# Kernel optimization log

Measured on AMD Instinct MI355X. Metric: run time of the kernel, lower is better.

Reference implementation:

```python
import jax, jax.numpy as jnp
import numpy as np

B, S, HID, H = 4, 1024, 1024, 16
D = HID // H


def setup_inputs() -> dict:
    key = jax.random.key(0)
    ks = jax.random.split(key, 4)
    scale = 0.02
    return {
        "hidden_states": jax.random.normal(ks[0], (B, S, HID), dtype=jnp.float32),
        "attention_mask": jnp.ones((B, S), dtype=jnp.int32),
        "layer_head_mask": jnp.ones((H,), dtype=jnp.float32),
        "Wq": jax.random.normal(ks[1], (HID, HID), dtype=jnp.float32) * scale,
        "bq": jnp.zeros((HID,), dtype=jnp.float32),
        "Wk": jax.random.normal(ks[2], (HID, HID), dtype=jnp.float32) * scale,
        "bk": jnp.zeros((HID,), dtype=jnp.float32),
        "Wv": jax.random.normal(ks[3], (HID, HID), dtype=jnp.float32) * scale,
        "bv": jnp.zeros((HID,), dtype=jnp.float32),
    }


def reference(hidden_states, attention_mask, layer_head_mask, Wq, bq, Wk, bk, Wv, bv):
    b, s, _ = hidden_states.shape
    # QKV projections, split heads: [B,S,H,D]
    q = (hidden_states @ Wq + bq).reshape(b, s, H, D)
    k = (hidden_states @ Wk + bk).reshape(b, s, H, D)
    v = (hidden_states @ Wv + bv).reshape(b, s, H, D)

    # attention bias from padding mask: [B,1,1,S]
    mask = attention_mask[:, None, None, :]
    neg = jnp.finfo(jnp.float32).min
    bias = jnp.where(mask > 0, 0.0, neg).astype(jnp.float32)

    # dot_product_attention_weights: scale query by 1/sqrt(D)
    q = q / jnp.sqrt(jnp.asarray(D, dtype=q.dtype))
    scores = jnp.einsum("bqhd,bkhd->bhqk", q, k) + bias  # [B,H,S,S]
    attn_weights = jax.nn.softmax(scores, axis=-1)

    # per-head masking
    attn_weights = attn_weights * layer_head_mask[None, :, None, None]

    attn_output = jnp.einsum("bhqk,bkhd->bqhd", attn_weights, v)
    return attn_output.reshape(b, s, HID)
```

## Files before the change

kernel.cpp:

```cpp
#include <hip/hip_runtime.h>
#include <stdint.h>

typedef __bf16 bf16_t;
typedef bf16_t __attribute__((ext_vector_type(8))) bf16x8;
typedef float __attribute__((ext_vector_type(4))) f32x4;
typedef float __attribute__((ext_vector_type(16))) f32x16;
typedef unsigned u32;

#define BATCH 4
#define SEQ 1024
#define HIDD 1024
#define NH 16
#define DH 64

__device__ __forceinline__ unsigned short f2bf(float f) {
  unsigned u = __float_as_uint(f);
  u += 0x7fffu + ((u >> 16) & 1u);
  return (unsigned short)(u >> 16);
}

__device__ __forceinline__ f32x4 mfma16(bf16x8 a, bf16x8 b, f32x4 c) {
  return __builtin_amdgcn_mfma_f32_16x16x32_bf16(a, b, c, 0, 0, 0);
}
__device__ __forceinline__ f32x16 mfma32(bf16x8 a, bf16x8 b, f32x16 c) {
  return __builtin_amdgcn_mfma_f32_32x32x16_bf16(a, b, c, 0, 0, 0);
}

__device__ __forceinline__ void gload_lds16(const void* g, void* l) {
  __builtin_amdgcn_global_load_lds(
      (__attribute__((address_space(1))) void*)(uintptr_t)g,
      (__attribute__((address_space(3))) void*)l, 16, 0, 0);
}

__device__ __forceinline__ u32 cvtpk(float lo, float hi) {
  u32 r;
  asm("v_cvt_pk_bf16_f32 %0, %1, %2" : "=v"(r) : "v"(lo), "v"(hi));
  return r;
}
__device__ __forceinline__ void plswap(u32& a, u32& b) {
  asm("v_permlane32_swap_b32 %0, %1" : "+v"(a), "+v"(b));
}

__global__ void hs2bf(const float* __restrict__ x, unsigned short* __restrict__ y) {
  const int i = blockIdx.x * 256 + threadIdx.x;
  const float4 f = ((const float4*)x)[i];
  ushort4 o = make_ushort4(f2bf(f.x), f2bf(f.y), f2bf(f.z), f2bf(f.w));
  ((ushort4*)y)[i] = o;
}

__global__ __launch_bounds__(256) void wtrans(
    const float* __restrict__ Wq, const float* __restrict__ Wk,
    const float* __restrict__ Wv, unsigned short* __restrict__ Wt) {
  __shared__ unsigned short tile[64][72];
  const int z = blockIdx.z;
  const float* W = (z == 0) ? Wq : (z == 1) ? Wk : Wv;
  unsigned short* o = Wt + (size_t)z * (1024 * 1024);
  const int k0 = blockIdx.x * 64, n0 = blockIdx.y * 64;
  const int r = threadIdx.x >> 6, c = threadIdx.x & 63;
#pragma unroll
  for (int i = 0; i < 16; ++i) {
    const int row = i * 4 + r;
    tile[row][c] = f2bf(W[(size_t)(k0 + row) * 1024 + n0 + c]);
  }
  __syncthreads();
#pragma unroll
  for (int i = 0; i < 16; ++i) {
    const int row = i * 4 + r;
    o[(size_t)(n0 + row) * 1024 + k0 + c] = tile[c][row];
  }
}

__global__ __launch_bounds__(256) void qkv_gemm(
    const unsigned short* __restrict__ A,
    const unsigned short* __restrict__ Wt,
    const float* __restrict__ bq, const float* __restrict__ bk,
    const float* __restrict__ bv,
    unsigned short* __restrict__ outb) {
  __shared__ alignas(16) unsigned short Alds[128 * 32];
  __shared__ alignas(16) unsigned short Blds[128 * 32];

  const int z = blockIdx.z;
  const unsigned short* Bt = Wt + (size_t)z * (1024 * 1024);
  const float* bias = (z == 0) ? bq : (z == 1) ? bk : bv;
  unsigned short* outp = outb + (size_t)z * (4096 * 1024);
  const float scale = (z == 0) ? 0.125f * 1.44269504089f : 1.0f;

  const int m0 = blockIdx.x * 128;
  const int n0 = blockIdx.y * 128;
  const int t = threadIdx.x;
  const int w = t >> 6, l = t & 63;
  const int lg = l >> 4, lc = l & 15;
  const int wr = w >> 1, wc = w & 1;

  f32x4 acc[4][4] = {};

  for (int kt = 0; kt < 1024; kt += 32) {
    __syncthreads();
#pragma unroll
    for (int i = 0; i < 2; ++i) {
      const int c = i * 256 + t;
      const int row = c >> 2;
      const int kp = (c & 3) * 8;
      gload_lds16(A + (size_t)(m0 + row) * 1024 + kt + kp,
                  (char*)Alds + i * 4096 + w * 1024);
      gload_lds16(Bt + (size_t)(n0 + row) * 1024 + kt + kp,
                  (char*)Blds + i * 4096 + w * 1024);
    }
    __syncthreads();

    bf16x8 af[4], bfr[4];
#pragma unroll
    for (int m = 0; m < 4; ++m)
      af[m] = *(const bf16x8*)(Alds + (wr * 64 + m * 16 + lc) * 32 + lg * 8);
#pragma unroll
    for (int n = 0; n < 4; ++n)
      bfr[n] = *(const bf16x8*)(Blds + (wc * 64 + n * 16 + lc) * 32 + lg * 8);
#pragma unroll
    for (int m = 0; m < 4; ++m)
#pragma unroll
      for (int n = 0; n < 4; ++n)
        acc[m][n] = mfma16(af[m], bfr[n], acc[m][n]);
  }

#pragma unroll
  for (int n = 0; n < 4; ++n) {
    const int col = n0 + wc * 64 + n * 16 + lc;
    const float bs = bias[col];
#pragma unroll
    for (int m = 0; m < 4; ++m)
#pragma unroll
      for (int r = 0; r < 4; ++r) {
        const int row = m0 + wr * 64 + m * 16 + lg * 4 + r;
        outp[(size_t)row * 1024 + col] = f2bf((acc[m][n][r] + bs) * scale);
      }
  }
}

__global__ __launch_bounds__(256) void kpack_kernel(
    const unsigned short* __restrict__ K, unsigned short* __restrict__ Kp) {
  const int kb = blockIdx.x, bh = blockIdx.y;
  const int b = bh >> 4, h = bh & 15;
  const int t = threadIdx.x, l = t & 63, s = t >> 6;
  const unsigned short* src = K + (size_t)(b * 1024 + kb * 32 + (l & 31)) * 1024 +
                              h * 64 + s * 16 + ((l >> 5) & 1) * 8;
  const uint4 v = *(const uint4*)src;
  *(uint4*)(Kp + ((size_t)(bh * 32 + kb) * 4 + s) * 512 + l * 8) = v;
}

__global__ __launch_bounds__(256) void vpack_kernel(
    const unsigned short* __restrict__ V, unsigned short* __restrict__ Vp) {
  __shared__ unsigned short tile[64][72];
  const int tt = blockIdx.x;
  const int hh = blockIdx.y;
  const int t = threadIdx.x;
#pragma unroll
  for (int i = 0; i < 2; ++i) {
    const int c = i * 256 + t;
    const int row = c >> 3, cp = c & 7;
    *(uint4*)&tile[row][cp * 8] =
        *(const uint4*)(V + (size_t)(tt * 64 + row) * 1024 + hh * 64 + cp * 8);
  }
  __syncthreads();
  const int b = tt >> 4, kt = tt & 15;
  const int bh = b * 16 + hh;
#pragma unroll
  for (int i = 0; i < 2; ++i) {
    const int c = i * 256 + t;
    const int l = c & 63, s = (c >> 6) & 3, g = c >> 8;
    const int kl = s * 16 + ((l >> 5) & 1) * 8;
    const int d = g * 32 + (l & 31);
    unsigned short buf[8];
#pragma unroll
    for (int e = 0; e < 8; ++e) buf[e] = tile[kl + e][d];
    *(uint4*)(Vp + ((size_t)(bh * 16 + kt) * 8 + g * 4 + s) * 512 + l * 8) =
        *(uint4*)buf;
  }
}

__global__ __launch_bounds__(256, 2) void attn_kernel(
    const unsigned short* __restrict__ Qb,
    const unsigned short* __restrict__ Kpack,
    const unsigned short* __restrict__ Vpack,
    const int* __restrict__ amask,
    const float* __restrict__ lhm,
    float* __restrict__ out) {
  __shared__ alignas(16) char K_lds[2][8192];
  __shared__ alignas(16) char V_lds[2][8192];

  const int id = blockIdx.x;
  const int swzid = (id & 7) * 64 + (id >> 3);
  const int qt = swzid & 7;
  const int bh = swzid >> 3;
  const int b = bh >> 4, h = bh & 15;
  const int t = threadIdx.x;
  const int w = t >> 6, l = t & 63;
  const int lo = l & 31, hi = l >> 5;
  const int q0 = qt * 128 + w * 32;

  const unsigned short* KpT = Kpack + (size_t)bh * 65536;
  const unsigned short* VpT = Vpack + (size_t)bh * 65536;
  const int soff = w * 512 + l * 8;

  const unsigned short* qp = Qb + (size_t)(b * SEQ + q0 + lo) * HIDD + h * DH + hi * 8;
  bf16x8 qf[4];
#pragma unroll
  for (int s = 0; s < 4; ++s) qf[s] = *(const bf16x8*)(qp + s * 16);

  bool needmask;
  {
    int andv = 1;
#pragma unroll
    for (int tkk = 0; tkk < 16; ++tkk)
      andv &= (amask[b * SEQ + tkk * 64 + l] > 0) ? 1 : 0;
    needmask = (__ballot(andv != 0) != ~0ull);
  }

  float m_run = -INFINITY, l_run = 0.f;
  f32x16 acc0 = {}, acc1 = {};

  auto stage = [&](int tk, int buf) {
    const unsigned short* ks = KpT + tk * 4096 + soff;
    const unsigned short* vs = VpT + tk * 4096 + soff;
    gload_lds16(ks, &K_lds[buf][w * 1024]);
    gload_lds16(ks + 2048, &K_lds[buf][4096 + w * 1024]);
    gload_lds16(vs, &V_lds[buf][w * 1024]);
    gload_lds16(vs + 2048, &V_lds[buf][4096 + w * 1024]);
  };

  stage(0, 0);

  for (int tk = 0; tk < 16; ++tk) {
    const int cur = tk & 1;

    if (tk < 15) {
      stage(tk + 1, cur ^ 1);
      asm volatile("s_waitcnt vmcnt(4)" ::: "memory");
    } else {
      asm volatile("s_waitcnt vmcnt(0)" ::: "memory");
    }
    __builtin_amdgcn_s_barrier();
    __builtin_amdgcn_sched_barrier(0);

    const char* kb = K_lds[cur];
    const char* vb = V_lds[cur];

    bf16x8 kf0[4], kf1[4], vf0[4], vf1[4];
#pragma unroll
    for (int s = 0; s < 4; ++s) {
      kf0[s] = *(const bf16x8*)(kb + s * 1024 + l * 16);
      kf1[s] = *(const bf16x8*)(kb + 4096 + s * 1024 + l * 16);
      vf0[s] = *(const bf16x8*)(vb + s * 1024 + l * 16);
      vf1[s] = *(const bf16x8*)(vb + 4096 + s * 1024 + l * 16);
    }

    f32x16 sg0 = {}, sg1 = {};
    __builtin_amdgcn_s_setprio(1);
#pragma unroll
    for (int s = 0; s < 4; ++s) {
      sg0 = mfma32(kf0[s], qf[s], sg0);
      sg1 = mfma32(kf1[s], qf[s], sg1);
    }
    __builtin_amdgcn_s_setprio(0);

    float t0[8];
#pragma unroll
    for (int i = 0; i < 8; ++i)
      t0[i] = fmaxf(fmaxf(sg0[i], sg0[i + 8]), fmaxf(sg1[i], sg1[i + 8]));
    float t1 = fmaxf(fmaxf(fmaxf(t0[0], t0[1]), fmaxf(t0[2], t0[3])),
                     fmaxf(fmaxf(t0[4], t0[5]), fmaxf(t0[6], t0[7])));
    const float pmax = fmaxf(t1, __shfl_xor(t1, 32));

    if (!__all(pmax <= m_run + 8.f)) {
      const float mnew = fmaxf(m_run, pmax);
      const float sc = __builtin_amdgcn_exp2f(m_run - mnew);
      m_run = mnew;
      l_run *= sc;
#pragma unroll
      for (int g = 0; g < 16; ++g) {
        const int rowi = (g & 3) + 8 * (g >> 2) + 4 * hi;
        const float scr = __shfl(sc, rowi);
        acc0[g] *= scr;
        acc1[g] *= scr;
      }
    }

#pragma unroll
    for (int g = 0; g < 16; ++g) {
      sg0[g] = __builtin_amdgcn_exp2f(sg0[g] - m_run);
      sg1[g] = __builtin_amdgcn_exp2f(sg1[g] - m_run);
    }

    if (needmask) {
      const int mv = amask[b * SEQ + tk * 64 + l];
      const unsigned long long m64 = __ballot(mv > 0);
      if (m64 != ~0ull) {
#pragma unroll
        for (int g = 0; g < 16; ++g) {
          const int krow = (g & 3) + 8 * (g >> 2) + 4 * hi;
          if (!((m64 >> krow) & 1)) sg0[g] = 0.f;
          if (!((m64 >> (krow + 32)) & 1)) sg1[g] = 0.f;
        }
      }
    }

    float s0[8];
#pragma unroll
    for (int i = 0; i < 8; ++i)
      s0[i] = (sg0[i] + sg0[i + 8]) + (sg1[i] + sg1[i + 8]);
    float rs = ((s0[0] + s0[1]) + (s0[2] + s0[3])) +
               ((s0[4] + s0[5]) + (s0[6] + s0[7]));
    rs += __shfl_xor(rs, 32);
    l_run += rs;

    auto mk = [](float a0, float a1, float a2, float a3,
                 float a4, float a5, float a6, float a7) -> bf16x8 {
      u32 x = cvtpk(a0, a1), y = cvtpk(a2, a3);
      u32 a = cvtpk(a4, a5), b2 = cvtpk(a6, a7);
      plswap(x, a);
      plswap(y, b2);
      union { u32 u[4]; bf16x8 v; } fu;
      fu.u[0] = x; fu.u[1] = y; fu.u[2] = a; fu.u[3] = b2;
      return fu.v;
    };
    const bf16x8 pa0 = mk(sg0[0], sg0[1], sg0[2], sg0[3], sg0[4], sg0[5], sg0[6], sg0[7]);
    const bf16x8 pa1 = mk(sg0[8], sg0[9], sg0[10], sg0[11], sg0[12], sg0[13], sg0[14], sg0[15]);
    const bf16x8 pa2 = mk(sg1[0], sg1[1], sg1[2], sg1[3], sg1[4], sg1[5], sg1[6], sg1[7]);
    const bf16x8 pa3 = mk(sg1[8], sg1[9], sg1[10], sg1[11], sg1[12], sg1[13], sg1[14], sg1[15]);

    __builtin_amdgcn_s_setprio(1);
#pragma unroll
    for (int s = 0; s < 4; ++s) {
      const bf16x8 paf = (s == 0) ? pa0 : (s == 1) ? pa1 : (s == 2) ? pa2 : pa3;
      acc0 = mfma32(paf, vf0[s], acc0);
      acc1 = mfma32(paf, vf1[s], acc1);
    }
    __builtin_amdgcn_s_setprio(0);

    __builtin_amdgcn_s_barrier();
  }

  const float hm = lhm[h];
  const float inv = hm / l_run;
  float* ob = out + (size_t)(b * SEQ + q0) * HIDD + h * DH + lo;
#pragma unroll
  for (int g = 0; g < 16; ++g) {
    const int rowi = (g & 3) + 8 * (g >> 2) + 4 * hi;
    const float iv = __shfl(inv, rowi);
    ob[(size_t)rowi * HIDD] = acc0[g] * iv;
    ob[(size_t)rowi * HIDD + 32] = acc1[g] * iv;
  }
}

extern "C" void kernel_launch(void* const* d_in, const int* in_sizes, int n_in,
                              void* d_out, int out_size, void* d_ws, size_t ws_size,
                              hipStream_t stream) {
  const float* hs = (const float*)d_in[0];
  const int* amask = (const int*)d_in[1];
  const float* lhm = (const float*)d_in[2];
  const float* Wq = (const float*)d_in[3];
  const float* bq = (const float*)d_in[4];
  const float* Wk = (const float*)d_in[5];
  const float* bk = (const float*)d_in[6];
  const float* Wv = (const float*)d_in[7];
  const float* bv = (const float*)d_in[8];
  float* out = (float*)d_out;

  char* ws = (char*)d_ws;
  unsigned short* HSbf = (unsigned short*)ws;
  unsigned short* Wt = (unsigned short*)(ws + (8u << 20));
  unsigned short* QKV = (unsigned short*)(ws + (14u << 20));
  unsigned short* Kpk = (unsigned short*)ws;
  unsigned short* Vpk = (unsigned short*)(ws + (38u << 20));

  hs2bf<<<4096, 256, 0, stream>>>(hs, HSbf);
  wtrans<<<dim3(16, 16, 3), 256, 0, stream>>>(Wq, Wk, Wv, Wt);
  qkv_gemm<<<dim3(32, 8, 3), 256, 0, stream>>>(HSbf, Wt, bq, bk, bv, QKV);
  kpack_kernel<<<dim3(32, 64), 256, 0, stream>>>(QKV + (size_t)4096 * 1024, Kpk);
  vpack_kernel<<<dim3(64, 16), 256, 0, stream>>>(QKV + (size_t)2 * 4096 * 1024, Vpk);
  attn_kernel<<<512, 256, 0, stream>>>(QKV, Kpk, Vpk, amask, lhm, out);
}
```

Before: 87.36 us.

## Fuse K/V packing into GEMM epilogue and software-pipeline QK^T with triple buffering

The QKV GEMM epilogue now writes K and V directly in the packed layouts the attention kernel consumes, which removes the separate kpack and vpack launches and their global round trip. The attention kernel moves to three LDS stages and computes the next tile's QK^T scores while the current tile's softmax and PV run, so score MFMAs overlap with the exp work. The risks are scattered 2-byte stores in the K/V epilogue, extra LDS use that could lower occupancy, and more register pressure from holding the next tile's K fragments.

```diff
diff --git a/kernel.cpp b/kernel.cpp
--- a/kernel.cpp
+++ b/kernel.cpp
@@ -75,14 +75,15 @@
     const unsigned short* __restrict__ Wt,
     const float* __restrict__ bq, const float* __restrict__ bk,
     const float* __restrict__ bv,
-    unsigned short* __restrict__ outb) {
+    unsigned short* __restrict__ Qb,
+    unsigned short* __restrict__ Kpk,
+    unsigned short* __restrict__ Vpk) {
   __shared__ alignas(16) unsigned short Alds[128 * 32];
   __shared__ alignas(16) unsigned short Blds[128 * 32];
 
   const int z = blockIdx.z;
   const unsigned short* Bt = Wt + (size_t)z * (1024 * 1024);
   const float* bias = (z == 0) ? bq : (z == 1) ? bk : bv;
-  unsigned short* outp = outb + (size_t)z * (4096 * 1024);
   const float scale = (z == 0) ? 0.125f * 1.44269504089f : 1.0f;
 
   const int m0 = blockIdx.x * 128;
@@ -122,58 +123,54 @@
         acc[m][n] = mfma16(af[m], bfr[n], acc[m][n]);
   }
 
-#pragma unroll
-  for (int n = 0; n < 4; ++n) {
-    const int col = n0 + wc * 64 + n * 16 + lc;
-    const float bs = bias[col];
-#pragma unroll
-    for (int m = 0; m < 4; ++m)
-#pragma unroll
-      for (int r = 0; r < 4; ++r) {
-        const int row = m0 + wr * 64 + m * 16 + lg * 4 + r;
-        outp[(size_t)row * 1024 + col] = f2bf((acc[m][n][r] + bs) * scale);
-      }
-  }
-}
-
-__global__ __launch_bounds__(256) void kpack_kernel(
-    const unsigned short* __restrict__ K, unsigned short* __restrict__ Kp) {
-  const int kb = blockIdx.x, bh = blockIdx.y;
-  const int b = bh >> 4, h = bh & 15;
-  const int t = threadIdx.x, l = t & 63, s = t >> 6;
-  const unsigned short* src = K + (size_t)(b * 1024 + kb * 32 + (l & 31)) * 1024 +
-                              h * 64 + s * 16 + ((l >> 5) & 1) * 8;
-  const uint4 v = *(const uint4*)src;
-  *(uint4*)(Kp + ((size_t)(bh * 32 + kb) * 4 + s) * 512 + l * 8) = v;
-}
-
-__global__ __launch_bounds__(256) void vpack_kernel(
-    const unsigned short* __restrict__ V, unsigned short* __restrict__ Vp) {
-  __shared__ unsigned short tile[64][72];
-  const int tt = blockIdx.x;
-  const int hh = blockIdx.y;
-  const int t = threadIdx.x;
-#pragma unroll
-  for (int i = 0; i < 2; ++i) {
-    const int c = i * 256 + t;
-    const int row = c >> 3, cp = c & 7;
-    *(uint4*)&tile[row][cp * 8] =
-        *(const uint4*)(V + (size_t)(tt * 64 + row) * 1024 + hh * 64 + cp * 8);
-  }
-  __syncthreads();
-  const int b = tt >> 4, kt = tt & 15;
-  const int bh = b * 16 + hh;
-#pragma unroll
-  for (int i = 0; i < 2; ++i) {
-    const int c = i * 256 + t;
-    const int l = c & 63, s = (c >> 6) & 3, g = c >> 8;
-    const int kl = s * 16 + ((l >> 5) & 1) * 8;
-    const int d = g * 32 + (l & 31);
-    unsigned short buf[8];
-#pragma unroll
-    for (int e = 0; e < 8; ++e) buf[e] = tile[kl + e][d];
-    *(uint4*)(Vp + ((size_t)(bh * 16 + kt) * 8 + g * 4 + s) * 512 + l * 8) =
-        *(uint4*)buf;
+  if (z == 0) {
+#pragma unroll
+    for (int n = 0; n < 4; ++n) {
+      const int col = n0 + wc * 64 + n * 16 + lc;
+      const float bs = bias[col];
+#pragma unroll
+      for (int m = 0; m < 4; ++m)
+#pragma unroll
+        for (int r = 0; r < 4; ++r) {
+          const int row = m0 + wr * 64 + m * 16 + lg * 4 + r;
+          Qb[(size_t)row * 1024 + col] = f2bf((acc[m][n][r] + bs) * scale);
+        }
+    }
+  } else if (z == 1) {
+#pragma unroll
+    for (int n = 0; n < 4; ++n) {
+      const int col = n0 + wc * 64 + n * 16 + lc;
+      const float bs = bias[col];
+      const int h = col >> 6, s = (col >> 4) & 3, hi = (col >> 3) & 1, e = col & 7;
+#pragma unroll
+      for (int m = 0; m < 4; ++m)
+#pragma unroll
+        for (int r = 0; r < 4; ++r) {
+          const int row = m0 + wr * 64 + m * 16 + lg * 4 + r;
+          const int bh = (row >> 10) * 16 + h, tl = row & 1023;
+          const int kb = tl >> 5, lo = tl & 31;
+          Kpk[(size_t)(((bh * 32 + kb) * 4 + s) * 512) + (lo + hi * 32) * 8 + e] =
+              f2bf(acc[m][n][r] + bs);
+        }
+    }
+  } else {
+#pragma unroll
+    for (int n = 0; n < 4; ++n) {
+      const int col = n0 + wc * 64 + n * 16 + lc;
+      const float bs = bias[col];
+      const int h = col >> 6, g = (col >> 5) & 1, lo = col & 31;
+#pragma unroll
+      for (int m = 0; m < 4; ++m)
+#pragma unroll
+        for (int r = 0; r < 4; ++r) {
+          const int row = m0 + wr * 64 + m * 16 + lg * 4 + r;
+          const int bh = (row >> 10) * 16 + h, tl = row & 1023;
+          const int kt = tl >> 6, within = tl & 63;
+          const int sv = within >> 4, hiv = (within >> 3) & 1, ev = within & 7;
+          Vpk[(size_t)(((bh * 16 + kt) * 8 + g * 4 + sv) * 512) +
+              (lo + hiv * 32) * 8 + ev] = f2bf(acc[m][n][r] + bs);
+        }
+    }
   }
 }
 
@@ -184,8 +181,8 @@
     const int* __restrict__ amask,
     const float* __restrict__ lhm,
     float* __restrict__ out) {
-  __shared__ alignas(16) char K_lds[2][8192];
-  __shared__ alignas(16) char V_lds[2][8192];
+  __shared__ alignas(16) char K_lds[3][8192];
+  __shared__ alignas(16) char V_lds[3][8192];
 
   const int id = blockIdx.x;
   const int swzid = (id & 7) * 64 + (id >> 3);
@@ -201,23 +198,6 @@
   const unsigned short* VpT = Vpack + (size_t)bh * 65536;
   const int soff = w * 512 + l * 8;
 
-  const unsigned short* qp = Qb + (size_t)(b * SEQ + q0 + lo) * HIDD + h * DH + hi * 8;
-  bf16x8 qf[4];
-#pragma unroll
-  for (int s = 0; s < 4; ++s) qf[s] = *(const bf16x8*)(qp + s * 16);
-
-  bool needmask;
-  {
-    int andv = 1;
-#pragma unroll
-    for (int tkk = 0; tkk < 16; ++tkk)
-      andv &= (amask[b * SEQ + tkk * 64 + l] > 0) ? 1 : 0;
-    needmask = (__ballot(andv != 0) != ~0ull);
-  }
-
-  float m_run = -INFINITY, l_run = 0.f;
-  f32x16 acc0 = {}, acc1 = {};
-
   auto stage = [&](int tk, int buf) {
     const unsigned short* ks = KpT + tk * 4096 + soff;
     const unsigned short* vs = VpT + tk * 4096 + soff;
@@ -227,40 +207,72 @@
     gload_lds16(vs + 2048, &V_lds[buf][4096 + w * 1024]);
   };
 
+  const unsigned short* qp = Qb + (size_t)(b * SEQ + q0 + lo) * HIDD + h * DH + hi * 8;
+  bf16x8 qf[4];
+#pragma unroll
+  for (int s = 0; s < 4; ++s) qf[s] = *(const bf16x8*)(qp + s * 16);
+
+  bool needmask;
+  {
+    int andv = 1;
+#pragma unroll
+    for (int tkk = 0; tkk < 16; ++tkk)
+      andv &= (amask[b * SEQ + tkk * 64 + l] > 0) ? 1 : 0;
+    needmask = (__ballot(andv != 0) != ~0ull);
+  }
+
   stage(0, 0);
+  stage(1, 1);
+  asm volatile("s_waitcnt vmcnt(4)" ::: "memory");
+  asm volatile("s_barrier" ::: "memory");
+
+  f32x16 sg0 = {}, sg1 = {};
+  {
+    const char* kb = K_lds[0];
+    bf16x8 kf0[4], kf1[4];
+#pragma unroll
+    for (int s = 0; s < 4; ++s) {
+      kf0[s] = *(const bf16x8*)(kb + s * 1024 + l * 16);
+      kf1[s] = *(const bf16x8*)(kb + 4096 + s * 1024 + l * 16);
+    }
+    __builtin_amdgcn_s_setprio(1);
+#pragma unroll
+    for (int s = 0; s < 4; ++s) {
+      sg0 = mfma32(kf0[s], qf[s], sg0);
+      sg1 = mfma32(kf1[s], qf[s], sg1);
+    }
+    __builtin_amdgcn_s_setprio(0);
+  }
+
+  float m_run = -INFINITY, l_run = 0.f;
+  f32x16 acc0 = {}, acc1 = {};
+  int c0 = 0, c1 = 1, c2 = 2;
 
   for (int tk = 0; tk < 16; ++tk) {
-    const int cur = tk & 1;
-
-    if (tk < 15) {
-      stage(tk + 1, cur ^ 1);
+    asm volatile("s_barrier" ::: "memory");
+    if (tk < 14) {
+      stage(tk + 2, c2);
       asm volatile("s_waitcnt vmcnt(4)" ::: "memory");
     } else {
       asm volatile("s_waitcnt vmcnt(0)" ::: "memory");
     }
-    __builtin_amdgcn_s_barrier();
-    __builtin_amdgcn_sched_barrier(0);
-
-    const char* kb = K_lds[cur];
-    const char* vb = V_lds[cur];
-
-    bf16x8 kf0[4], kf1[4], vf0[4], vf1[4];
+
+    const char* vb = V_lds[c0];
+    bf16x8 vf0[4], vf1[4];
 #pragma unroll
     for (int s = 0; s < 4; ++s) {
-      kf0[s] = *(const bf16x8*)(kb + s * 1024 + l * 16);
-      kf1[s] = *(const bf16x8*)(kb + 4096 + s * 1024 + l * 16);
       vf0[s] = *(const bf16x8*)(vb + s * 1024 + l * 16);
       vf1[s] = *(const bf16x8*)(vb + 4096 + s * 1024 + l * 16);
     }
-
-    f32x16 sg0 = {}, sg1 = {};
-    __builtin_amdgcn_s_setprio(1);
-#pragma unroll
-    for (int s = 0; s < 4; ++s) {
-      sg0 = mfma32(kf0[s], qf[s], sg0);
-      sg1 = mfma32(kf1[s], qf[s], sg1);
-    }
-    __builtin_amdgcn_s_setprio(0);
+    bf16x8 nk0[4], nk1[4];
+    if (tk < 15) {
+      const char* kb = K_lds[c1];
+#pragma unroll
+      for (int s = 0; s < 4; ++s) {
+        nk0[s] = *(const bf16x8*)(kb + s * 1024 + l * 16);
+        nk1[s] = *(const bf16x8*)(kb + 4096 + s * 1024 + l * 16);
+      }
+    }
 
     float t0[8];
 #pragma unroll
@@ -336,7 +348,20 @@
     }
     __builtin_amdgcn_s_setprio(0);
 
-    __builtin_amdgcn_s_barrier();
+    if (tk < 15) {
+      f32x16 a = {}, b2 = {};
+      __builtin_amdgcn_s_setprio(1);
+#pragma unroll
+      for (int s = 0; s < 4; ++s) {
+        a = mfma32(nk0[s], qf[s], a);
+        b2 = mfma32(nk1[s], qf[s], b2);
+      }
+      __builtin_amdgcn_s_setprio(0);
+      sg0 = a;
+      sg1 = b2;
+    }
+
+    const int tmp = c0; c0 = c1; c1 = c2; c2 = tmp;
   }
 
   const float hm = lhm[h];
@@ -368,14 +393,12 @@
   char* ws = (char*)d_ws;
   unsigned short* HSbf = (unsigned short*)ws;
   unsigned short* Wt = (unsigned short*)(ws + (8u << 20));
-  unsigned short* QKV = (unsigned short*)(ws + (14u << 20));
-  unsigned short* Kpk = (unsigned short*)ws;
-  unsigned short* Vpk = (unsigned short*)(ws + (38u << 20));
+  unsigned short* Qb = (unsigned short*)(ws + (14u << 20));
+  unsigned short* Kpk = (unsigned short*)(ws + (22u << 20));
+  unsigned short* Vpk = (unsigned short*)(ws + (30u << 20));
 
   hs2bf<<<4096, 256, 0, stream>>>(hs, HSbf);
   wtrans<<<dim3(16, 16, 3), 256, 0, stream>>>(Wq, Wk, Wv, Wt);
-  qkv_gemm<<<dim3(32, 8, 3), 256, 0, stream>>>(HSbf, Wt, bq, bk, bv, QKV);
-  kpack_kernel<<<dim3(32, 64), 256, 0, stream>>>(QKV + (size_t)4096 * 1024, Kpk);
-  vpack_kernel<<<dim3(64, 16), 256, 0, stream>>>(QKV + (size_t)2 * 4096 * 1024, Vpk);
-  attn_kernel<<<512, 256, 0, stream>>>(QKV, Kpk, Vpk, amask, lhm, out);
-}
+  qkv_gemm<<<dim3(32, 8, 3), 256, 0, stream>>>(HSbf, Wt, bq, bk, bv, Qb, Kpk, Vpk);
+  attn_kernel<<<512, 256, 0, stream>>>(Qb, Kpk, Vpk, amask, lhm, out);
+}
```

New measurement: 88.52 us. About the same (+1.3%).
